# Kernel optimization log

Hardware: AMD Instinct MI355X
Metric: run time of the kernel (lower is better)

The kernel has to match this reference:

```python
import jax, jax.numpy as jnp
import numpy as np

H = 768   # config.hidden_size
B = 1024  # batch
S = 256   # attention context length
C1, C2, C3 = 202, 183, 11  # num_class for crit, law, time


def setup_inputs() -> dict:
    key = jax.random.key(0)
    ks = jax.random.split(key, 18)
    sd = 1.0 / np.sqrt(H)
    def u(k, shape):
        return jax.random.uniform(k, shape, jnp.float32, -sd, sd)
    return {
        "x": jax.random.normal(ks[0], (B, H), jnp.float32),
        "attn": jax.random.normal(ks[1], (B, S, H), jnp.float32),
        # 3 LSTMCells (tasks crit, law, time), stacked
        "Wih": u(ks[2], (3, 4 * H, H)),
        "Whh": u(ks[3], (3, 4 * H, H)),
        "bih": u(ks[4], (3, 4 * H)),
        "bhh": u(ks[5], (3, 4 * H)),
        # edge (2->3) hidden/cell state Linear (only edge whose FC is reached)
        "hfc_W": u(ks[6], (H, H)), "hfc_b": u(ks[7], (H,)),
        "cfc_W": u(ks[8], (H, H)), "cfc_b": u(ks[9], (H,)),
        # midfc per task
        "midfc_W": u(ks[10], (3, H, H)), "midfc_b": u(ks[11], (3, H)),
        # outfc per task (distinct class counts)
        "out1_W": u(ks[12], (C1, H)), "out1_b": u(ks[13], (C1,)),
        "out2_W": u(ks[14], (C2, H)), "out2_b": u(ks[15], (C2,)),
        "out3_W": u(ks[16], (C3, H)), "out3_b": u(ks[17], (C3,)),
    }


def _lstm_cell(x, h, c, Wih, Whh, bih, bhh):
    # torch nn.LSTMCell: gate order i, f, g, o
    gates = x @ Wih.T + bih + h @ Whh.T + bhh
    i, f, g, o = jnp.split(gates, 4, axis=-1)
    c_new = jax.nn.sigmoid(f) * c + jax.nn.sigmoid(i) * jnp.tanh(g)
    h_new = jax.nn.sigmoid(o) * jnp.tanh(c_new)
    return h_new, c_new


def _attend(h, attn):
    # Attention: ratio = softmax(bmm(attn, h)); result = bmm(attn^T, ratio)
    w = jax.nn.softmax(jnp.einsum('bsh,bh->bs', attn, h), axis=1)
    return jnp.einsum('bsh,bs->bh', attn, w)


def _head(h, mW, mb, oW, ob):
    # more_fc=True: outfc(relu(midfc(h)))
    return jax.nn.relu(h @ mW.T + mb) @ oW.T + ob


def reference(x, attn, Wih, Whh, bih, bhh, hfc_W, hfc_b, cfc_W, cfc_b,
              midfc_W, midfc_b, out1_W, out1_b, out2_W, out2_b, out3_W, out3_b):
    # graph "[(1 2),(1 3),(2 3)]": edges 1->2, 1->3, 2->3; initial hidden_list all zero.
    z = jnp.zeros_like(x)
    # task 1 (crit): runs on zero state; first-touch sets hidden[2]=hidden[3]=(h1,c1)
    h1, c1 = _lstm_cell(x, z, z, Wih[0], Whh[0], bih[0], bhh[0])
    # task 2 (law): state = (h1, c1)
    h2, c2 = _lstm_cell(x, h1, c1, Wih[1], Whh[1], bih[1], bhh[1])
    # edge 2->3 applies the per-edge Linear and accumulates into hidden[3]
    hp3 = h1 + h2 @ hfc_W.T + hfc_b
    cp3 = c1 + c2 @ cfc_W.T + cfc_b
    # task 3 (time)
    h3, c3 = _lstm_cell(x, hp3, cp3, Wih[2], Whh[2], bih[2], bhh[2])
    # attention over encoder context, per task head
    a1 = _attend(h1, attn)
    a2 = _attend(h2, attn)
    a3 = _attend(h3, attn)
    o1 = _head(a1, midfc_W[0], midfc_b[0], out1_W, out1_b)
    o2 = _head(a2, midfc_W[1], midfc_b[1], out2_W, out2_b)
    o3 = _head(a3, midfc_W[2], midfc_b[2], out3_W, out3_b)
    return (o1, o2, o3)
```

## Files before the change

### kernel.cpp

```cpp
#include <hip/hip_runtime.h>


typedef unsigned short u16;
typedef _Float16       f16x8 __attribute__((ext_vector_type(8)));
typedef float          f32x4 __attribute__((ext_vector_type(4)));

#define SWZ(r) ((((r) + ((r) >> 2))) & 3)

__device__ __forceinline__ u16 f2h(float f) {
  _Float16 h = (_Float16)f;
  return __builtin_bit_cast(u16, h);
}
__device__ __forceinline__ float sigm(float x) { return 1.f / (1.f + __expf(-x)); }
__device__ __forceinline__ float ftanh(float x) { return 1.f - 2.f / (__expf(2.f * x) + 1.f); }

__device__ __forceinline__ void gld16(const u16* g, u16* l) {
  __builtin_amdgcn_global_load_lds(
      (const __attribute__((address_space(1))) unsigned int*)(g),
      (__attribute__((address_space(3))) unsigned int*)(l),
      16, 0, 0);
}

struct GJob {
  const u16* A; const u16* W;
  float* outf; u16* outh;
  const float* bias; const float* bias2; const float* addend;
  int N; int ldc; int relu;
};
struct GArgs { GJob j[3]; };

__global__ __launch_bounds__(256)
void gemm_k(GArgs P, int K)
{
  const GJob jb = P.j[blockIdx.z];
  const int bn0 = blockIdx.x * 128;
  if (bn0 >= jb.N) return;
  const int bm0 = blockIdx.y * 64;

  __shared__ __align__(16) u16 As[2][64 * 32];
  __shared__ __align__(16) u16 Bs[2][128 * 32];

  const int tid = threadIdx.x, lane = tid & 63, wv = tid >> 6;

  const int ra  = tid >> 2,        csa  = (tid & 3) ^ SWZ(ra);
  const int rb0 = tid >> 2,        csb0 = (tid & 3) ^ SWZ(rb0);
  const int rb1 = (tid >> 2) + 64, csb1 = (tid & 3) ^ SWZ(rb1);
  int wr0 = bn0 + rb0; if (wr0 >= jb.N) wr0 = jb.N - 1;
  int wr1 = bn0 + rb1; if (wr1 >= jb.N) wr1 = jb.N - 1;
  const u16* gA  = jb.A + (size_t)(bm0 + ra) * K + csa * 8;
  const u16* gB0 = jb.W + (size_t)wr0 * K + csb0 * 8;
  const u16* gB1 = jb.W + (size_t)wr1 * K + csb1 * 8;

  const int frow = lane & 15, fsl = lane >> 4;

  f32x4 acc[8];
#pragma unroll
  for (int n = 0; n < 8; ++n) acc[n] = (f32x4){0.f, 0.f, 0.f, 0.f};

  const int NT = K >> 5;
  gld16(gA,  &As[0][wv * 512]);
  gld16(gB0, &Bs[0][wv * 512]);
  gld16(gB1, &Bs[0][2048 + wv * 512]);
  __syncthreads();

  for (int it = 0; it < NT; ++it) {
    const int cur = it & 1, nxt = cur ^ 1;
    if (it + 1 < NT) {
      const int k0 = (it + 1) * 32;
      gld16(gA + k0,  &As[nxt][wv * 512]);
      gld16(gB0 + k0, &Bs[nxt][wv * 512]);
      gld16(gB1 + k0, &Bs[nxt][2048 + wv * 512]);
    }
    f16x8 ah, bh[8];
    {
      const int ar = wv * 16 + frow;
      ah = *(const f16x8*)(&As[cur][ar * 32 + ((fsl ^ SWZ(ar)) * 8)]);
    }
#pragma unroll
    for (int n = 0; n < 8; ++n) {
      const int br = n * 16 + frow;
      bh[n] = *(const f16x8*)(&Bs[cur][br * 32 + ((fsl ^ SWZ(br)) * 8)]);
    }
#pragma unroll
    for (int n = 0; n < 8; ++n)
      acc[n] = __builtin_amdgcn_mfma_f32_16x16x32_f16(ah, bh[n], acc[n], 0, 0, 0);
    __syncthreads();
  }

  const int rb = (lane >> 4) * 4;
  const int cc = lane & 15;
#pragma unroll
  for (int n = 0; n < 8; ++n) {
    const int col = bn0 + n * 16 + cc;
    if (col >= jb.N) continue;
    float bv = 0.f;
    if (jb.bias)  bv += jb.bias[col];
    if (jb.bias2) bv += jb.bias2[col];
    const int row0 = bm0 + wv * 16 + rb;
#pragma unroll
    for (int r = 0; r < 4; ++r) {
      const int row = row0 + r;
      float v = acc[n][r] + bv;
      if (jb.addend) v += jb.addend[(size_t)row * jb.ldc + col];
      if (jb.relu)   v = fmaxf(v, 0.f);
      if (jb.outf)   jb.outf[(size_t)row * jb.ldc + col] = v;
      if (jb.outh)   jb.outh[(size_t)row * jb.ldc + col] = f2h(v);
    }
  }
}

__global__ __launch_bounds__(256)
void cell_k(const u16* __restrict__ A, const u16* __restrict__ W,
            const float* __restrict__ bi, const float* __restrict__ bh_,
            const float* __restrict__ addend, int lda,
            const float* __restrict__ cprev,
            float* __restrict__ hf, float* __restrict__ cf,
            u16* __restrict__ hh, u16* __restrict__ ch, int K)
{
  const int bj0 = blockIdx.x * 32;
  const int bm0 = blockIdx.y * 64;

  __shared__ __align__(16) u16 As[2][64 * 32];
  __shared__ __align__(16) u16 Bs[2][128 * 32];

  const int tid = threadIdx.x, lane = tid & 63, wv = tid >> 6;

  const int ra  = tid >> 2,        csa  = (tid & 3) ^ SWZ(ra);
  const int rb0 = tid >> 2,        csb0 = (tid & 3) ^ SWZ(rb0);
  const int rb1 = (tid >> 2) + 64, csb1 = (tid & 3) ^ SWZ(rb1);
  const int wr0 = (rb0 >> 5) * 768 + bj0 + (rb0 & 31);
  const int wr1 = (rb1 >> 5) * 768 + bj0 + (rb1 & 31);
  const u16* gA  = A + (size_t)(bm0 + ra) * K + csa * 8;
  const u16* gB0 = W + (size_t)wr0 * K + csb0 * 8;
  const u16* gB1 = W + (size_t)wr1 * K + csb1 * 8;

  const int frow = lane & 15, fsl = lane >> 4;

  f32x4 acc[8];
#pragma unroll
  for (int n = 0; n < 8; ++n) acc[n] = (f32x4){0.f, 0.f, 0.f, 0.f};

  const int NT = K >> 5;
  gld16(gA,  &As[0][wv * 512]);
  gld16(gB0, &Bs[0][wv * 512]);
  gld16(gB1, &Bs[0][2048 + wv * 512]);
  __syncthreads();

  for (int it = 0; it < NT; ++it) {
    const int cur = it & 1, nxt = cur ^ 1;
    if (it + 1 < NT) {
      const int k0 = (it + 1) * 32;
      gld16(gA + k0,  &As[nxt][wv * 512]);
      gld16(gB0 + k0, &Bs[nxt][wv * 512]);
      gld16(gB1 + k0, &Bs[nxt][2048 + wv * 512]);
    }
    f16x8 ah, bh8[8];
    {
      const int ar = wv * 16 + frow;
      ah = *(const f16x8*)(&As[cur][ar * 32 + ((fsl ^ SWZ(ar)) * 8)]);
    }
#pragma unroll
    for (int n = 0; n < 8; ++n) {
      const int br = n * 16 + frow;
      bh8[n] = *(const f16x8*)(&Bs[cur][br * 32 + ((fsl ^ SWZ(br)) * 8)]);
    }
#pragma unroll
    for (int n = 0; n < 8; ++n)
      acc[n] = __builtin_amdgcn_mfma_f32_16x16x32_f16(ah, bh8[n], acc[n], 0, 0, 0);
    __syncthreads();
  }

  const int rb = (lane >> 4) * 4;
  const int cc = lane & 15;
#pragma unroll
  for (int jj = 0; jj < 2; ++jj) {
    const int j = bj0 + jj * 16 + cc;
    float b_i = 0.f, b_f = 0.f, b_g = 0.f, b_o = 0.f;
    if (bi) {
      b_i = bi[j]        + bh_[j];
      b_f = bi[768 + j]  + bh_[768 + j];
      b_g = bi[1536 + j] + bh_[1536 + j];
      b_o = bi[2304 + j] + bh_[2304 + j];
    }
    const int row0 = bm0 + wv * 16 + rb;
#pragma unroll
    for (int r = 0; r < 4; ++r) {
      const int row = row0 + r;
      float gi = acc[0 + jj][r] + b_i;
      float gf = acc[2 + jj][r] + b_f;
      float gg = acc[4 + jj][r] + b_g;
      float go = acc[6 + jj][r] + b_o;
      if (addend) {
        const float* ad = addend + (size_t)row * lda;
        gi += ad[j]; gf += ad[768 + j]; gg += ad[1536 + j]; go += ad[2304 + j];
      }
      float c = sigm(gi) * ftanh(gg);
      if (cprev) c += sigm(gf) * cprev[row * 768 + j];
      float h = sigm(go) * ftanh(c);
      if (hf) hf[row * 768 + j] = h;
      if (cf) cf[row * 768 + j] = c;
      if (hh) hh[row * 768 + j] = f2h(h);
      if (ch) ch[row * 768 + j] = f2h(c);
    }
  }
}

struct CvtArgs {
  const float* src[9];
  u16*         dst[9];
  int n[9];
  int pfx[10];
};

__global__ __launch_bounds__(256)
void cvt_k(CvtArgs a)
{
  int blk = blockIdx.x, s = 0;
  while (s < 8 && blk >= a.pfx[s + 1]) ++s;
  int idx = ((blk - a.pfx[s]) * 256 + (int)threadIdx.x) * 4;
  if (idx >= a.n[s]) return;
  float4 v = *(const float4*)(a.src[s] + idx);
  ushort4 h;
  h.x = f2h(v.x); h.y = f2h(v.y); h.z = f2h(v.z); h.w = f2h(v.w);
  *(ushort4*)(a.dst[s] + idx) = h;
}

__global__ __launch_bounds__(256)
void attn_k(const float* __restrict__ attn,
            const float* __restrict__ h1, const float* __restrict__ h2,
            const float* __restrict__ h3,
            u16* __restrict__ a1, u16* __restrict__ a2, u16* __restrict__ a3)
{
  const int b = blockIdx.x, tid = threadIdx.x;
  const int lane = tid & 63, wv = tid >> 6;
  __shared__ float accW[4][3][768];
  __shared__ float lsumW[4][3];

  const float* ab = attn + (size_t)b * 256 * 768;
  const int cb = lane * 4;

  float4 hh[3][3];
#pragma unroll
  for (int j = 0; j < 3; ++j) {
    hh[0][j] = *(const float4*)(h1 + b * 768 + j * 256 + cb);
    hh[1][j] = *(const float4*)(h2 + b * 768 + j * 256 + cb);
    hh[2][j] = *(const float4*)(h3 + b * 768 + j * 256 + cb);
  }

  float4 acc[3][3];
#pragma unroll
  for (int t3 = 0; t3 < 3; ++t3)
#pragma unroll
    for (int j = 0; j < 3; ++j) acc[t3][j] = (float4){0.f, 0.f, 0.f, 0.f};
  float lsum[3] = {0.f, 0.f, 0.f};

  const int row0 = wv * 64;
  for (int sub = 0; sub < 16; ++sub) {
    const float* rp = ab + (size_t)(row0 + sub * 4) * 768 + cb;
    float4 vv[4][3];
#pragma unroll
    for (int s = 0; s < 4; ++s)
#pragma unroll
      for (int j = 0; j < 3; ++j)
        vv[s][j] = *(const float4*)(rp + s * 768 + j * 256);

    float q[3][4];
#pragma unroll
    for (int t3 = 0; t3 < 3; ++t3)
#pragma unroll
      for (int s = 0; s < 4; ++s) {
        float d = 0.f;
#pragma unroll
        for (int j = 0; j < 3; ++j) {
          d = fmaf(vv[s][j].x, hh[t3][j].x, d);
          d = fmaf(vv[s][j].y, hh[t3][j].y, d);
          d = fmaf(vv[s][j].z, hh[t3][j].z, d);
          d = fmaf(vv[s][j].w, hh[t3][j].w, d);
        }
        q[t3][s] = d;
      }
#pragma unroll
    for (int t3 = 0; t3 < 3; ++t3)
#pragma unroll
      for (int s = 0; s < 4; ++s) {
#pragma unroll
        for (int d = 1; d < 64; d <<= 1)
          q[t3][s] += __shfl_xor(q[t3][s], d);
        q[t3][s] = __expf(q[t3][s]);
      }
#pragma unroll
    for (int t3 = 0; t3 < 3; ++t3)
#pragma unroll
      for (int s = 0; s < 4; ++s) {
        const float p = q[t3][s];
        lsum[t3] += p;
#pragma unroll
        for (int j = 0; j < 3; ++j) {
          acc[t3][j].x = fmaf(p, vv[s][j].x, acc[t3][j].x);
          acc[t3][j].y = fmaf(p, vv[s][j].y, acc[t3][j].y);
          acc[t3][j].z = fmaf(p, vv[s][j].z, acc[t3][j].z);
          acc[t3][j].w = fmaf(p, vv[s][j].w, acc[t3][j].w);
        }
      }
  }

#pragma unroll
  for (int t3 = 0; t3 < 3; ++t3)
#pragma unroll
    for (int j = 0; j < 3; ++j)
      *(float4*)(&accW[wv][t3][j * 256 + cb]) = acc[t3][j];
  if (lane == 0) {
#pragma unroll
    for (int t3 = 0; t3 < 3; ++t3) lsumW[wv][t3] = lsum[t3];
  }
  __syncthreads();

  float ltot[3];
#pragma unroll
  for (int t3 = 0; t3 < 3; ++t3)
    ltot[t3] = lsumW[0][t3] + lsumW[1][t3] + lsumW[2][t3] + lsumW[3][t3];
  u16* outs[3] = { a1, a2, a3 };
#pragma unroll
  for (int cc = 0; cc < 3; ++cc) {
    const int c = tid + cc * 256;
#pragma unroll
    for (int t3 = 0; t3 < 3; ++t3) {
      float s = accW[0][t3][c] + accW[1][t3][c] + accW[2][t3][c] + accW[3][t3][c];
      outs[t3][b * 768 + c] = f2h(s / ltot[t3]);
    }
  }
}

extern "C" void kernel_launch(void* const* d_in, const int* in_sizes, int n_in,
                              void* d_out, int out_size, void* d_ws, size_t ws_size,
                              hipStream_t stream)
{
  const float* x    = (const float*)d_in[0];
  const float* attn = (const float*)d_in[1];
  const float* Wih  = (const float*)d_in[2];
  const float* Whh  = (const float*)d_in[3];
  const float* bih  = (const float*)d_in[4];
  const float* bhh  = (const float*)d_in[5];
  const float* hfcW = (const float*)d_in[6];
  const float* hfcb = (const float*)d_in[7];
  const float* cfcW = (const float*)d_in[8];
  const float* cfcb = (const float*)d_in[9];
  const float* midW = (const float*)d_in[10];
  const float* midb = (const float*)d_in[11];
  const float* o1W  = (const float*)d_in[12];
  const float* o1b  = (const float*)d_in[13];
  const float* o2W  = (const float*)d_in[14];
  const float* o2b  = (const float*)d_in[15];
  const float* o3W  = (const float*)d_in[16];
  const float* o3b  = (const float*)d_in[17];
  float* out = (float*)d_out;
  char*  ws  = (char*)d_ws;

  float* Gpre = (float*)(ws + 0);
  float* h1f  = (float*)(ws + 25165824);
  float* c1f  = (float*)(ws + 28311552);
  float* h2f  = (float*)(ws + 31457280);
  float* cp3f = (float*)(ws + 34603008);
  float* h3f  = (float*)(ws + 37748736);
  u16*   xh   = (u16*)(ws + 40894464);
  u16*   Wihh = (u16*)(ws + 42467328);
  u16*   Whhh = (u16*)(ws + 56623104);
  u16*   hfch = (u16*)(ws + 66060288);
  u16*   cfch = (u16*)(ws + 67239936);
  u16*   midh = (u16*)(ws + 68419584);
  u16*   o1h  = (u16*)(ws + 71958528);
  u16*   o2h  = (u16*)(ws + 72268800);
  u16*   o3h  = (u16*)(ws + 72549888);
  u16*   h1h  = (u16*)(ws + 72566784);
  u16*   h2h  = (u16*)(ws + 74139648);
  u16*   c2h  = (u16*)(ws + 75712512);
  u16*   hp3h = (u16*)(ws + 77285376);
  u16*   a1h  = (u16*)(ws + 78858240);
  u16*   a2h  = (u16*)(ws + 80431104);
  u16*   a3h  = (u16*)(ws + 82003968);
  u16*   m1h  = (u16*)(ws + 83576832);
  u16*   m2h  = (u16*)(ws + 85149696);
  u16*   m3h  = (u16*)(ws + 86722560);

  CvtArgs ca;
  const float* srcs[9] = { x, Wih, Whh + 2359296, hfcW, cfcW, midW, o1W, o2W, o3W };
  u16*         dsts[9] = { xh, Wihh, Whhh, hfch, cfch, midh, o1h, o2h, o3h };
  int ns[9] = { 786432, 7077888, 4718592, 589824, 589824, 1769472, 155136, 140544, 8448 };
  int pfx = 0;
  for (int i = 0; i < 9; ++i) {
    ca.src[i] = srcs[i]; ca.dst[i] = dsts[i]; ca.n[i] = ns[i];
    ca.pfx[i] = pfx; pfx += (ns[i] + 1023) / 1024;
  }
  ca.pfx[9] = pfx;
  cvt_k<<<pfx, 256, 0, stream>>>(ca);

  GArgs P;

  P = GArgs{};
  P.j[0] = { xh, Wihh + (size_t)3072 * 768, Gpre, nullptr,
             bih + 3072, bhh + 3072, nullptr, 6144, 6144, 0 };
  gemm_k<<<dim3(48, 16, 1), 256, 0, stream>>>(P, 768);

  cell_k<<<dim3(24, 16), 256, 0, stream>>>(xh, Wihh, bih, bhh,
      nullptr, 0, nullptr, h1f, c1f, h1h, nullptr, 768);

  cell_k<<<dim3(24, 16), 256, 0, stream>>>(h1h, Whhh, nullptr, nullptr,
      Gpre, 6144, c1f, h2f, nullptr, h2h, c2h, 768);

  P = GArgs{};
  P.j[0] = { h2h, hfch, nullptr, hp3h, hfcb, nullptr, h1f, 768, 768, 0 };
  P.j[1] = { c2h, cfch, cp3f, nullptr, cfcb, nullptr, c1f, 768, 768, 0 };
  gemm_k<<<dim3(6, 16, 2), 256, 0, stream>>>(P, 768);

  cell_k<<<dim3(24, 16), 256, 0, stream>>>(hp3h, Whhh + 2359296, nullptr, nullptr,
      Gpre + 3072, 6144, cp3f, h3f, nullptr, nullptr, nullptr, 768);

  attn_k<<<1024, 256, 0, stream>>>(attn, h1f, h2f, h3f, a1h, a2h, a3h);

  P = GArgs{};
  P.j[0] = { a1h, midh,           nullptr, m1h, midb,        nullptr, nullptr, 768, 768, 1 };
  P.j[1] = { a2h, midh +  589824, nullptr, m2h, midb +  768, nullptr, nullptr, 768, 768, 1 };
  P.j[2] = { a3h, midh + 1179648, nullptr, m3h, midb + 1536, nullptr, nullptr, 768, 768, 1 };
  gemm_k<<<dim3(6, 16, 3), 256, 0, stream>>>(P, 768);

  P = GArgs{};
  P.j[0] = { m1h, o1h, out,          nullptr, o1b, nullptr, nullptr, 202, 202, 0 };
  P.j[1] = { m2h, o2h, out + 206848, nullptr, o2b, nullptr, nullptr, 183, 183, 0 };
  P.j[2] = { m3h, o3h, out + 394240, nullptr, o3b, nullptr, nullptr,  11,  11, 0 };
  gemm_k<<<dim3(2, 16, 3), 256, 0, stream>>>(P, 768);

  (void)in_sizes; (void)n_in; (void)out_size; (void)ws_size;
}
```

Baseline: 348.9 us.

## Fuse input and recurrent GEMMs into cell kernels with 4-stage LDS pipeline

Removes the separate precomputed x@Wih gate GEMM for tasks 2 and 3. Each cell kernel now accumulates both x@Wih and h@Whh over a concatenated K of 1536, which avoids writing and re-reading a 25 MB fp32 gate buffer. The K loop in both the GEMM and cell kernels moves from double buffering to a 4-buffer LDS ring with three tiles in flight, using explicit vmcnt waits and raw barriers. The cost is more LDS per block (48 KB), which may reduce occupancy, and the cell kernels for tasks 2 and 3 now do twice the K work each.

```diff
diff --git a/kernel.cpp b/kernel.cpp
--- a/kernel.cpp
+++ b/kernel.cpp
@@ -6,6 +6,8 @@
 typedef float          f32x4 __attribute__((ext_vector_type(4)));
 
 #define SWZ(r) ((((r) + ((r) >> 2))) & 3)
+#define VMCNT(N) asm volatile("s_waitcnt vmcnt(" #N ")" ::: "memory")
+#define KBAR()  do { __builtin_amdgcn_s_barrier(); __builtin_amdgcn_sched_barrier(0); } while (0)
 
 __device__ __forceinline__ u16 f2h(float f) {
   _Float16 h = (_Float16)f;
@@ -20,6 +22,54 @@
       (__attribute__((address_space(3))) unsigned int*)(l),
       16, 0, 0);
 }
+
+struct KP { const u16 *pA1, *pA2, *pW1_0, *pW2_0, *pW1_1, *pW2_1; };
+
+__device__ __forceinline__ void stage_tile(const KP& kp, int kt, int ntA,
+                                           u16* Asb, u16* Bsb, int wv) {
+  const bool s1 = (kt < ntA);
+  const int off = (s1 ? kt : kt - ntA) * 32;
+  gld16((s1 ? kp.pA1  : kp.pA2 ) + off, Asb + wv * 512);
+  gld16((s1 ? kp.pW1_0 : kp.pW2_0) + off, Bsb + wv * 512);
+  gld16((s1 ? kp.pW1_1 : kp.pW2_1) + off, Bsb + 2048 + wv * 512);
+}
+
+__device__ __forceinline__ void compute_tile(const u16* Asb, const u16* Bsb,
+                                             int wv, int frow, int fsl, f32x4* acc) {
+  const int ar = wv * 16 + frow;
+  f16x8 ah = *(const f16x8*)(Asb + ar * 32 + ((fsl ^ SWZ(ar)) * 8));
+  f16x8 bh[8];
+#pragma unroll
+  for (int n = 0; n < 8; ++n) {
+    const int br = n * 16 + frow;
+    bh[n] = *(const f16x8*)(Bsb + br * 32 + ((fsl ^ SWZ(br)) * 8));
+  }
+#pragma unroll
+  for (int n = 0; n < 8; ++n)
+    acc[n] = __builtin_amdgcn_mfma_f32_16x16x32_f16(ah, bh[n], acc[n], 0, 0, 0);
+}
+
+#define KLOOP(kp, ntA, NT, As, Bs, wv, frow, fsl, acc)                          \
+  do {                                                                          \
+    stage_tile(kp, 0, ntA, As, Bs, wv);                                         \
+    stage_tile(kp, 1, ntA, As + 2048, Bs + 4096, wv);                           \
+    stage_tile(kp, 2, ntA, As + 4096, Bs + 8192, wv);                           \
+    for (int t = 0; t < NT - 2; ++t) {                                          \
+      VMCNT(6); KBAR();                                                         \
+      const int cb = t & 3;                                                     \
+      compute_tile(As + cb * 2048, Bs + cb * 4096, wv, frow, fsl, acc);         \
+      if (t + 3 < NT) {                                                         \
+        const int sb = (t + 3) & 3;                                             \
+        stage_tile(kp, t + 3, ntA, As + sb * 2048, Bs + sb * 4096, wv);         \
+      }                                                                         \
+    }                                                                           \
+    VMCNT(3); KBAR();                                                           \
+    compute_tile(As + ((NT - 2) & 3) * 2048, Bs + ((NT - 2) & 3) * 4096,        \
+                 wv, frow, fsl, acc);                                           \
+    VMCNT(0); KBAR();                                                           \
+    compute_tile(As + ((NT - 1) & 3) * 2048, Bs + ((NT - 1) & 3) * 4096,        \
+                 wv, frow, fsl, acc);                                           \
+  } while (0)
 
 struct GJob {
   const u16* A; const u16* W;
@@ -30,62 +80,35 @@
 struct GArgs { GJob j[3]; };
 
 __global__ __launch_bounds__(256)
-void gemm_k(GArgs P, int K)
+void gemm_k(GArgs P)
 {
   const GJob jb = P.j[blockIdx.z];
   const int bn0 = blockIdx.x * 128;
   if (bn0 >= jb.N) return;
   const int bm0 = blockIdx.y * 64;
 
-  __shared__ __align__(16) u16 As[2][64 * 32];
-  __shared__ __align__(16) u16 Bs[2][128 * 32];
+  __shared__ __align__(16) u16 As[4 * 64 * 32];
+  __shared__ __align__(16) u16 Bs[4 * 128 * 32];
 
   const int tid = threadIdx.x, lane = tid & 63, wv = tid >> 6;
+  const int frow = lane & 15, fsl = lane >> 4;
 
   const int ra  = tid >> 2,        csa  = (tid & 3) ^ SWZ(ra);
   const int rb0 = tid >> 2,        csb0 = (tid & 3) ^ SWZ(rb0);
   const int rb1 = (tid >> 2) + 64, csb1 = (tid & 3) ^ SWZ(rb1);
   int wr0 = bn0 + rb0; if (wr0 >= jb.N) wr0 = jb.N - 1;
   int wr1 = bn0 + rb1; if (wr1 >= jb.N) wr1 = jb.N - 1;
-  const u16* gA  = jb.A + (size_t)(bm0 + ra) * K + csa * 8;
-  const u16* gB0 = jb.W + (size_t)wr0 * K + csb0 * 8;
-  const u16* gB1 = jb.W + (size_t)wr1 * K + csb1 * 8;
-
-  const int frow = lane & 15, fsl = lane >> 4;
+
+  KP kp;
+  kp.pA1 = kp.pA2 = jb.A + (size_t)(bm0 + ra) * 768 + csa * 8;
+  kp.pW1_0 = kp.pW2_0 = jb.W + (size_t)wr0 * 768 + csb0 * 8;
+  kp.pW1_1 = kp.pW2_1 = jb.W + (size_t)wr1 * 768 + csb1 * 8;
 
   f32x4 acc[8];
 #pragma unroll
   for (int n = 0; n < 8; ++n) acc[n] = (f32x4){0.f, 0.f, 0.f, 0.f};
 
-  const int NT = K >> 5;
-  gld16(gA,  &As[0][wv * 512]);
-  gld16(gB0, &Bs[0][wv * 512]);
-  gld16(gB1, &Bs[0][2048 + wv * 512]);
-  __syncthreads();
-
-  for (int it = 0; it < NT; ++it) {
-    const int cur = it & 1, nxt = cur ^ 1;
-    if (it + 1 < NT) {
-      const int k0 = (it + 1) * 32;
-      gld16(gA + k0,  &As[nxt][wv * 512]);
-      gld16(gB0 + k0, &Bs[nxt][wv * 512]);
-      gld16(gB1 + k0, &Bs[nxt][2048 + wv * 512]);
-    }
-    f16x8 ah, bh[8];
-    {
-      const int ar = wv * 16 + frow;
-      ah = *(const f16x8*)(&As[cur][ar * 32 + ((fsl ^ SWZ(ar)) * 8)]);
-    }
-#pragma unroll
-    for (int n = 0; n < 8; ++n) {
-      const int br = n * 16 + frow;
-      bh[n] = *(const f16x8*)(&Bs[cur][br * 32 + ((fsl ^ SWZ(br)) * 8)]);
-    }
-#pragma unroll
-    for (int n = 0; n < 8; ++n)
-      acc[n] = __builtin_amdgcn_mfma_f32_16x16x32_f16(ah, bh[n], acc[n], 0, 0, 0);
-    __syncthreads();
-  }
+  KLOOP(kp, 24, 24, As, Bs, wv, frow, fsl, acc);
 
   const int rb = (lane >> 4) * 4;
   const int cc = lane & 15;
@@ -110,78 +133,51 @@
 }
 
 __global__ __launch_bounds__(256)
-void cell_k(const u16* __restrict__ A, const u16* __restrict__ W,
+void cell_k(const u16* __restrict__ A1, const u16* __restrict__ A2,
+            const u16* __restrict__ W1, const u16* __restrict__ W2,
             const float* __restrict__ bi, const float* __restrict__ bh_,
-            const float* __restrict__ addend, int lda,
             const float* __restrict__ cprev,
             float* __restrict__ hf, float* __restrict__ cf,
-            u16* __restrict__ hh, u16* __restrict__ ch, int K)
+            u16* __restrict__ hh, u16* __restrict__ ch, int NT)
 {
   const int bj0 = blockIdx.x * 32;
   const int bm0 = blockIdx.y * 64;
 
-  __shared__ __align__(16) u16 As[2][64 * 32];
-  __shared__ __align__(16) u16 Bs[2][128 * 32];
+  __shared__ __align__(16) u16 As[4 * 64 * 32];
+  __shared__ __align__(16) u16 Bs[4 * 128 * 32];
 
   const int tid = threadIdx.x, lane = tid & 63, wv = tid >> 6;
+  const int frow = lane & 15, fsl = lane >> 4;
 
   const int ra  = tid >> 2,        csa  = (tid & 3) ^ SWZ(ra);
   const int rb0 = tid >> 2,        csb0 = (tid & 3) ^ SWZ(rb0);
   const int rb1 = (tid >> 2) + 64, csb1 = (tid & 3) ^ SWZ(rb1);
   const int wr0 = (rb0 >> 5) * 768 + bj0 + (rb0 & 31);
   const int wr1 = (rb1 >> 5) * 768 + bj0 + (rb1 & 31);
-  const u16* gA  = A + (size_t)(bm0 + ra) * K + csa * 8;
-  const u16* gB0 = W + (size_t)wr0 * K + csb0 * 8;
-  const u16* gB1 = W + (size_t)wr1 * K + csb1 * 8;
-
-  const int frow = lane & 15, fsl = lane >> 4;
+
+  KP kp;
+  kp.pA1  = A1 + (size_t)(bm0 + ra) * 768 + csa * 8;
+  kp.pA2  = A2 + (size_t)(bm0 + ra) * 768 + csa * 8;
+  kp.pW1_0 = W1 + (size_t)wr0 * 768 + csb0 * 8;
+  kp.pW2_0 = W2 + (size_t)wr0 * 768 + csb0 * 8;
+  kp.pW1_1 = W1 + (size_t)wr1 * 768 + csb1 * 8;
+  kp.pW2_1 = W2 + (size_t)wr1 * 768 + csb1 * 8;
 
   f32x4 acc[8];
 #pragma unroll
   for (int n = 0; n < 8; ++n) acc[n] = (f32x4){0.f, 0.f, 0.f, 0.f};
 
-  const int NT = K >> 5;
-  gld16(gA,  &As[0][wv * 512]);
-  gld16(gB0, &Bs[0][wv * 512]);
-  gld16(gB1, &Bs[0][2048 + wv * 512]);
-  __syncthreads();
-
-  for (int it = 0; it < NT; ++it) {
-    const int cur = it & 1, nxt = cur ^ 1;
-    if (it + 1 < NT) {
-      const int k0 = (it + 1) * 32;
-      gld16(gA + k0,  &As[nxt][wv * 512]);
-      gld16(gB0 + k0, &Bs[nxt][wv * 512]);
-      gld16(gB1 + k0, &Bs[nxt][2048 + wv * 512]);
-    }
-    f16x8 ah, bh8[8];
-    {
-      const int ar = wv * 16 + frow;
-      ah = *(const f16x8*)(&As[cur][ar * 32 + ((fsl ^ SWZ(ar)) * 8)]);
-    }
-#pragma unroll
-    for (int n = 0; n < 8; ++n) {
-      const int br = n * 16 + frow;
-      bh8[n] = *(const f16x8*)(&Bs[cur][br * 32 + ((fsl ^ SWZ(br)) * 8)]);
-    }
-#pragma unroll
-    for (int n = 0; n < 8; ++n)
-      acc[n] = __builtin_amdgcn_mfma_f32_16x16x32_f16(ah, bh8[n], acc[n], 0, 0, 0);
-    __syncthreads();
-  }
+  KLOOP(kp, 24, NT, As, Bs, wv, frow, fsl, acc);
 
   const int rb = (lane >> 4) * 4;
   const int cc = lane & 15;
 #pragma unroll
   for (int jj = 0; jj < 2; ++jj) {
     const int j = bj0 + jj * 16 + cc;
-    float b_i = 0.f, b_f = 0.f, b_g = 0.f, b_o = 0.f;
-    if (bi) {
-      b_i = bi[j]        + bh_[j];
-      b_f = bi[768 + j]  + bh_[768 + j];
-      b_g = bi[1536 + j] + bh_[1536 + j];
-      b_o = bi[2304 + j] + bh_[2304 + j];
-    }
+    const float b_i = bi[j]        + bh_[j];
+    const float b_f = bi[768 + j]  + bh_[768 + j];
+    const float b_g = bi[1536 + j] + bh_[1536 + j];
+    const float b_o = bi[2304 + j] + bh_[2304 + j];
     const int row0 = bm0 + wv * 16 + rb;
 #pragma unroll
     for (int r = 0; r < 4; ++r) {
@@ -190,10 +186,6 @@
       float gf = acc[2 + jj][r] + b_f;
       float gg = acc[4 + jj][r] + b_g;
       float go = acc[6 + jj][r] + b_o;
-      if (addend) {
-        const float* ad = addend + (size_t)row * lda;
-        gi += ad[j]; gf += ad[768 + j]; gg += ad[1536 + j]; go += ad[2304 + j];
-      }
       float c = sigm(gi) * ftanh(gg);
       if (cprev) c += sigm(gf) * cprev[row * 768 + j];
       float h = sigm(go) * ftanh(c);
@@ -356,31 +348,30 @@
   float* out = (float*)d_out;
   char*  ws  = (char*)d_ws;
 
-  float* Gpre = (float*)(ws + 0);
-  float* h1f  = (float*)(ws + 25165824);
-  float* c1f  = (float*)(ws + 28311552);
-  float* h2f  = (float*)(ws + 31457280);
-  float* cp3f = (float*)(ws + 34603008);
-  float* h3f  = (float*)(ws + 37748736);
-  u16*   xh   = (u16*)(ws + 40894464);
-  u16*   Wihh = (u16*)(ws + 42467328);
-  u16*   Whhh = (u16*)(ws + 56623104);
-  u16*   hfch = (u16*)(ws + 66060288);
-  u16*   cfch = (u16*)(ws + 67239936);
-  u16*   midh = (u16*)(ws + 68419584);
-  u16*   o1h  = (u16*)(ws + 71958528);
-  u16*   o2h  = (u16*)(ws + 72268800);
-  u16*   o3h  = (u16*)(ws + 72549888);
-  u16*   h1h  = (u16*)(ws + 72566784);
-  u16*   h2h  = (u16*)(ws + 74139648);
-  u16*   c2h  = (u16*)(ws + 75712512);
-  u16*   hp3h = (u16*)(ws + 77285376);
-  u16*   a1h  = (u16*)(ws + 78858240);
-  u16*   a2h  = (u16*)(ws + 80431104);
-  u16*   a3h  = (u16*)(ws + 82003968);
-  u16*   m1h  = (u16*)(ws + 83576832);
-  u16*   m2h  = (u16*)(ws + 85149696);
-  u16*   m3h  = (u16*)(ws + 86722560);
+  float* h1f  = (float*)(ws + 0);
+  float* c1f  = (float*)(ws + 3145728);
+  float* h2f  = (float*)(ws + 6291456);
+  float* cp3f = (float*)(ws + 9437184);
+  float* h3f  = (float*)(ws + 12582912);
+  u16*   xh   = (u16*)(ws + 15728640);
+  u16*   Wihh = (u16*)(ws + 17301504);
+  u16*   Whhh = (u16*)(ws + 31457280);
+  u16*   hfch = (u16*)(ws + 40894464);
+  u16*   cfch = (u16*)(ws + 42074112);
+  u16*   midh = (u16*)(ws + 43253760);
+  u16*   o1h  = (u16*)(ws + 46792704);
+  u16*   o2h  = (u16*)(ws + 47102976);
+  u16*   o3h  = (u16*)(ws + 47384064);
+  u16*   h1h  = (u16*)(ws + 47400960);
+  u16*   h2h  = (u16*)(ws + 48973824);
+  u16*   c2h  = (u16*)(ws + 50546688);
+  u16*   hp3h = (u16*)(ws + 52119552);
+  u16*   a1h  = (u16*)(ws + 53692416);
+  u16*   a2h  = (u16*)(ws + 55265280);
+  u16*   a3h  = (u16*)(ws + 56838144);
+  u16*   m1h  = (u16*)(ws + 58411008);
+  u16*   m2h  = (u16*)(ws + 59983872);
+  u16*   m3h  = (u16*)(ws + 61556736);
 
   CvtArgs ca;
   const float* srcs[9] = { x, Wih, Whh + 2359296, hfcW, cfcW, midW, o1W, o2W, o3W };
@@ -396,24 +387,21 @@
 
   GArgs P;
 
-  P = GArgs{};
-  P.j[0] = { xh, Wihh + (size_t)3072 * 768, Gpre, nullptr,
-             bih + 3072, bhh + 3072, nullptr, 6144, 6144, 0 };
-  gemm_k<<<dim3(48, 16, 1), 256, 0, stream>>>(P, 768);
-
-  cell_k<<<dim3(24, 16), 256, 0, stream>>>(xh, Wihh, bih, bhh,
-      nullptr, 0, nullptr, h1f, c1f, h1h, nullptr, 768);
-
-  cell_k<<<dim3(24, 16), 256, 0, stream>>>(h1h, Whhh, nullptr, nullptr,
-      Gpre, 6144, c1f, h2f, nullptr, h2h, c2h, 768);
+  cell_k<<<dim3(24, 16), 256, 0, stream>>>(xh, xh, Wihh, Wihh,
+      bih, bhh, nullptr, h1f, c1f, h1h, nullptr, 24);
+
+  cell_k<<<dim3(24, 16), 256, 0, stream>>>(xh, h1h,
+      Wihh + (size_t)3072 * 768, Whhh,
+      bih + 3072, bhh + 3072, c1f, h2f, nullptr, h2h, c2h, 48);
 
   P = GArgs{};
   P.j[0] = { h2h, hfch, nullptr, hp3h, hfcb, nullptr, h1f, 768, 768, 0 };
   P.j[1] = { c2h, cfch, cp3f, nullptr, cfcb, nullptr, c1f, 768, 768, 0 };
-  gemm_k<<<dim3(6, 16, 2), 256, 0, stream>>>(P, 768);
-
-  cell_k<<<dim3(24, 16), 256, 0, stream>>>(hp3h, Whhh + 2359296, nullptr, nullptr,
-      Gpre + 3072, 6144, cp3f, h3f, nullptr, nullptr, nullptr, 768);
+  gemm_k<<<dim3(6, 16, 2), 256, 0, stream>>>(P);
+
+  cell_k<<<dim3(24, 16), 256, 0, stream>>>(xh, hp3h,
+      Wihh + (size_t)6144 * 768, Whhh + 2359296,
+      bih + 6144, bhh + 6144, cp3f, h3f, nullptr, nullptr, nullptr, 48);
 
   attn_k<<<1024, 256, 0, stream>>>(attn, h1f, h2f, h3f, a1h, a2h, a3h);
 
@@ -421,13 +409,13 @@
   P.j[0] = { a1h, midh,           nullptr, m1h, midb,        nullptr, nullptr, 768, 768, 1 };
   P.j[1] = { a2h, midh +  589824, nullptr, m2h, midb +  768, nullptr, nullptr, 768, 768, 1 };
   P.j[2] = { a3h, midh + 1179648, nullptr, m3h, midb + 1536, nullptr, nullptr, 768, 768, 1 };
-  gemm_k<<<dim3(6, 16, 3), 256, 0, stream>>>(P, 768);
+  gemm_k<<<dim3(6, 16, 3), 256, 0, stream>>>(P);
 
   P = GArgs{};
   P.j[0] = { m1h, o1h, out,          nullptr, o1b, nullptr, nullptr, 202, 202, 0 };
   P.j[1] = { m2h, o2h, out + 206848, nullptr, o2b, nullptr, nullptr, 183, 183, 0 };
   P.j[2] = { m3h, o3h, out + 394240, nullptr, o3b, nullptr, nullptr,  11,  11, 0 };
-  gemm_k<<<dim3(2, 16, 3), 256, 0, stream>>>(P, 768);
+  gemm_k<<<dim3(2, 16, 3), 256, 0, stream>>>(P);
 
   (void)in_sizes; (void)n_in; (void)out_size; (void)ws_size;
 }
```

Result: faster. 323.1 us (-7.4%).

## Deepen GEMM pipeline to four LDS stages and fuse first-stage kernels

Applied to the files above, without the earlier changes.

The shared GEMM main loop now uses a four-buffer LDS ring with three tiles in flight. It waits with explicit vmcnt counters and raw barriers instead of double buffering with a __syncthreads per tile. The conversion kernel is split in two: x and Wih are converted first, then one fused kernel runs cell 1, the Wih gate precompute GEMM and the remaining weight conversions as separate block ranges. This removes launches and overlaps conversion with compute. K is now hardcoded to 768 and LDS use per block doubles, which may lower occupancy.

```diff
diff --git a/kernel.cpp b/kernel.cpp
--- a/kernel.cpp
+++ b/kernel.cpp
@@ -6,6 +6,8 @@
 typedef float          f32x4 __attribute__((ext_vector_type(4)));
 
 #define SWZ(r) ((((r) + ((r) >> 2))) & 3)
+#define VMCNT(N) asm volatile("s_waitcnt vmcnt(" #N ")" ::: "memory")
+#define KBAR()  do { __builtin_amdgcn_s_barrier(); __builtin_amdgcn_sched_barrier(0); } while (0)
 
 __device__ __forceinline__ u16 f2h(float f) {
   _Float16 h = (_Float16)f;
@@ -19,6 +21,54 @@
       (const __attribute__((address_space(1))) unsigned int*)(g),
       (__attribute__((address_space(3))) unsigned int*)(l),
       16, 0, 0);
+}
+
+struct KP { const u16 *pA, *pW0, *pW1; };
+
+__device__ __forceinline__ void stage_tile(const KP& kp, int kt,
+                                           u16* Asb, u16* Bsb, int wv) {
+  const int off = kt * 32;
+  gld16(kp.pA  + off, Asb + wv * 512);
+  gld16(kp.pW0 + off, Bsb + wv * 512);
+  gld16(kp.pW1 + off, Bsb + 2048 + wv * 512);
+}
+
+__device__ __forceinline__ void compute_tile(const u16* Asb, const u16* Bsb,
+                                             int wv, int frow, int fsl, f32x4* acc) {
+  const int ar = wv * 16 + frow;
+  f16x8 ah = *(const f16x8*)(Asb + ar * 32 + ((fsl ^ SWZ(ar)) * 8));
+  f16x8 bh[8];
+#pragma unroll
+  for (int n = 0; n < 8; ++n) {
+    const int br = n * 16 + frow;
+    bh[n] = *(const f16x8*)(Bsb + br * 32 + ((fsl ^ SWZ(br)) * 8));
+  }
+#pragma unroll
+  for (int n = 0; n < 8; ++n)
+    acc[n] = __builtin_amdgcn_mfma_f32_16x16x32_f16(ah, bh[n], acc[n], 0, 0, 0);
+}
+
+__device__ __forceinline__ void kloop(const KP& kp, u16* As, u16* Bs,
+                                      int wv, int frow, int fsl, f32x4* acc) {
+  const int NT = 24;
+  stage_tile(kp, 0, As,        Bs,        wv);
+  stage_tile(kp, 1, As + 2048, Bs + 4096, wv);
+  stage_tile(kp, 2, As + 4096, Bs + 8192, wv);
+  for (int t = 0; t < NT - 2; ++t) {
+    VMCNT(6); KBAR();
+    const int cb = t & 3;
+    compute_tile(As + cb * 2048, Bs + cb * 4096, wv, frow, fsl, acc);
+    if (t + 3 < NT) {
+      const int sb = (t + 3) & 3;
+      stage_tile(kp, t + 3, As + sb * 2048, Bs + sb * 4096, wv);
+    }
+  }
+  VMCNT(3); KBAR();
+  compute_tile(As + ((NT - 2) & 3) * 2048, Bs + ((NT - 2) & 3) * 4096,
+               wv, frow, fsl, acc);
+  VMCNT(0); KBAR();
+  compute_tile(As + ((NT - 1) & 3) * 2048, Bs + ((NT - 1) & 3) * 4096,
+               wv, frow, fsl, acc);
 }
 
 struct GJob {
@@ -27,65 +77,30 @@
   const float* bias; const float* bias2; const float* addend;
   int N; int ldc; int relu;
 };
-struct GArgs { GJob j[3]; };
-
-__global__ __launch_bounds__(256)
-void gemm_k(GArgs P, int K)
-{
-  const GJob jb = P.j[blockIdx.z];
-  const int bn0 = blockIdx.x * 128;
+
+__device__ __forceinline__ void run_gemm(const GJob& jb, int bx, int by,
+                                         u16* As, u16* Bs, int tid) {
+  const int bn0 = bx * 128;
   if (bn0 >= jb.N) return;
-  const int bm0 = blockIdx.y * 64;
-
-  __shared__ __align__(16) u16 As[2][64 * 32];
-  __shared__ __align__(16) u16 Bs[2][128 * 32];
-
-  const int tid = threadIdx.x, lane = tid & 63, wv = tid >> 6;
+  const int bm0 = by * 64;
+  const int lane = tid & 63, wv = tid >> 6;
+  const int frow = lane & 15, fsl = lane >> 4;
 
   const int ra  = tid >> 2,        csa  = (tid & 3) ^ SWZ(ra);
-  const int rb0 = tid >> 2,        csb0 = (tid & 3) ^ SWZ(rb0);
   const int rb1 = (tid >> 2) + 64, csb1 = (tid & 3) ^ SWZ(rb1);
-  int wr0 = bn0 + rb0; if (wr0 >= jb.N) wr0 = jb.N - 1;
+  int wr0 = bn0 + ra;  if (wr0 >= jb.N) wr0 = jb.N - 1;
   int wr1 = bn0 + rb1; if (wr1 >= jb.N) wr1 = jb.N - 1;
-  const u16* gA  = jb.A + (size_t)(bm0 + ra) * K + csa * 8;
-  const u16* gB0 = jb.W + (size_t)wr0 * K + csb0 * 8;
-  const u16* gB1 = jb.W + (size_t)wr1 * K + csb1 * 8;
-
-  const int frow = lane & 15, fsl = lane >> 4;
+
+  KP kp;
+  kp.pA  = jb.A + (size_t)(bm0 + ra) * 768 + csa * 8;
+  kp.pW0 = jb.W + (size_t)wr0 * 768 + csa * 8;
+  kp.pW1 = jb.W + (size_t)wr1 * 768 + csb1 * 8;
 
   f32x4 acc[8];
 #pragma unroll
   for (int n = 0; n < 8; ++n) acc[n] = (f32x4){0.f, 0.f, 0.f, 0.f};
 
-  const int NT = K >> 5;
-  gld16(gA,  &As[0][wv * 512]);
-  gld16(gB0, &Bs[0][wv * 512]);
-  gld16(gB1, &Bs[0][2048 + wv * 512]);
-  __syncthreads();
-
-  for (int it = 0; it < NT; ++it) {
-    const int cur = it & 1, nxt = cur ^ 1;
-    if (it + 1 < NT) {
-      const int k0 = (it + 1) * 32;
-      gld16(gA + k0,  &As[nxt][wv * 512]);
-      gld16(gB0 + k0, &Bs[nxt][wv * 512]);
-      gld16(gB1 + k0, &Bs[nxt][2048 + wv * 512]);
-    }
-    f16x8 ah, bh[8];
-    {
-      const int ar = wv * 16 + frow;
-      ah = *(const f16x8*)(&As[cur][ar * 32 + ((fsl ^ SWZ(ar)) * 8)]);
-    }
-#pragma unroll
-    for (int n = 0; n < 8; ++n) {
-      const int br = n * 16 + frow;
-      bh[n] = *(const f16x8*)(&Bs[cur][br * 32 + ((fsl ^ SWZ(br)) * 8)]);
-    }
-#pragma unroll
-    for (int n = 0; n < 8; ++n)
-      acc[n] = __builtin_amdgcn_mfma_f32_16x16x32_f16(ah, bh[n], acc[n], 0, 0, 0);
-    __syncthreads();
-  }
+  kloop(kp, As, Bs, wv, frow, fsl, acc);
 
   const int rb = (lane >> 4) * 4;
   const int cc = lane & 15;
@@ -109,66 +124,33 @@
   }
 }
 
-__global__ __launch_bounds__(256)
-void cell_k(const u16* __restrict__ A, const u16* __restrict__ W,
-            const float* __restrict__ bi, const float* __restrict__ bh_,
-            const float* __restrict__ addend, int lda,
-            const float* __restrict__ cprev,
-            float* __restrict__ hf, float* __restrict__ cf,
-            u16* __restrict__ hh, u16* __restrict__ ch, int K)
-{
-  const int bj0 = blockIdx.x * 32;
-  const int bm0 = blockIdx.y * 64;
-
-  __shared__ __align__(16) u16 As[2][64 * 32];
-  __shared__ __align__(16) u16 Bs[2][128 * 32];
-
-  const int tid = threadIdx.x, lane = tid & 63, wv = tid >> 6;
+__device__ __forceinline__ void run_cell(const u16* A, const u16* W,
+                                         const float* bi, const float* bh_,
+                                         const float* addend,
+                                         const float* cprev,
+                                         float* hf, float* cf, u16* hh, u16* ch,
+                                         int bx, int by,
+                                         u16* As, u16* Bs, int tid) {
+  const int bj0 = bx * 32;
+  const int bm0 = by * 64;
+  const int lane = tid & 63, wv = tid >> 6;
+  const int frow = lane & 15, fsl = lane >> 4;
 
   const int ra  = tid >> 2,        csa  = (tid & 3) ^ SWZ(ra);
-  const int rb0 = tid >> 2,        csb0 = (tid & 3) ^ SWZ(rb0);
   const int rb1 = (tid >> 2) + 64, csb1 = (tid & 3) ^ SWZ(rb1);
-  const int wr0 = (rb0 >> 5) * 768 + bj0 + (rb0 & 31);
+  const int wr0 = (ra >> 5) * 768 + bj0 + (ra & 31);
   const int wr1 = (rb1 >> 5) * 768 + bj0 + (rb1 & 31);
-  const u16* gA  = A + (size_t)(bm0 + ra) * K + csa * 8;
-  const u16* gB0 = W + (size_t)wr0 * K + csb0 * 8;
-  const u16* gB1 = W + (size_t)wr1 * K + csb1 * 8;
-
-  const int frow = lane & 15, fsl = lane >> 4;
+
+  KP kp;
+  kp.pA  = A + (size_t)(bm0 + ra) * 768 + csa * 8;
+  kp.pW0 = W + (size_t)wr0 * 768 + csa * 8;
+  kp.pW1 = W + (size_t)wr1 * 768 + csb1 * 8;
 
   f32x4 acc[8];
 #pragma unroll
   for (int n = 0; n < 8; ++n) acc[n] = (f32x4){0.f, 0.f, 0.f, 0.f};
 
-  const int NT = K >> 5;
-  gld16(gA,  &As[0][wv * 512]);
-  gld16(gB0, &Bs[0][wv * 512]);
-  gld16(gB1, &Bs[0][2048 + wv * 512]);
-  __syncthreads();
-
-  for (int it = 0; it < NT; ++it) {
-    const int cur = it & 1, nxt = cur ^ 1;
-    if (it + 1 < NT) {
-      const int k0 = (it + 1) * 32;
-      gld16(gA + k0,  &As[nxt][wv * 512]);
-      gld16(gB0 + k0, &Bs[nxt][wv * 512]);
-      gld16(gB1 + k0, &Bs[nxt][2048 + wv * 512]);
-    }
-    f16x8 ah, bh8[8];
-    {
-      const int ar = wv * 16 + frow;
-      ah = *(const f16x8*)(&As[cur][ar * 32 + ((fsl ^ SWZ(ar)) * 8)]);
-    }
-#pragma unroll
-    for (int n = 0; n < 8; ++n) {
-      const int br = n * 16 + frow;
-      bh8[n] = *(const f16x8*)(&Bs[cur][br * 32 + ((fsl ^ SWZ(br)) * 8)]);
-    }
-#pragma unroll
-    for (int n = 0; n < 8; ++n)
-      acc[n] = __builtin_amdgcn_mfma_f32_16x16x32_f16(ah, bh8[n], acc[n], 0, 0, 0);
-    __syncthreads();
-  }
+  kloop(kp, As, Bs, wv, frow, fsl, acc);
 
   const int rb = (lane >> 4) * 4;
   const int cc = lane & 15;
@@ -191,7 +173,7 @@
       float gg = acc[4 + jj][r] + b_g;
       float go = acc[6 + jj][r] + b_o;
       if (addend) {
-        const float* ad = addend + (size_t)row * lda;
+        const float* ad = addend + (size_t)row * 6144;
         gi += ad[j]; gf += ad[768 + j]; gg += ad[1536 + j]; go += ad[2304 + j];
       }
       float c = sigm(gi) * ftanh(gg);
@@ -205,24 +187,79 @@
   }
 }
 
-struct CvtArgs {
-  const float* src[9];
-  u16*         dst[9];
-  int n[9];
-  int pfx[10];
+__device__ __forceinline__ void cvt_seg(const float* s, u16* d, int n4,
+                                        int gtid, int nthr) {
+  for (int i = gtid; i < n4; i += nthr) {
+    float4 v = ((const float4*)s)[i];
+    ushort4 h;
+    h.x = f2h(v.x); h.y = f2h(v.y); h.z = f2h(v.z); h.w = f2h(v.w);
+    ((ushort4*)d)[i] = h;
+  }
+}
+
+__global__ __launch_bounds__(256)
+void cvt0_k(const float* x, u16* xh, const float* Wih, u16* Wihh)
+{
+  const int g = blockIdx.x * 256 + threadIdx.x, N = 2048 * 256;
+  cvt_seg(x,   xh,   196608,  g, N);
+  cvt_seg(Wih, Wihh, 1769472, g, N);
+}
+
+struct K1P {
+  const u16 *xh, *Wihh;
+  const float *bih, *bhh;
+  float *h1f, *c1f; u16* h1h;
+  float* Gpre;
+  const float *Whh, *hfcW, *cfcW, *midW, *o1W, *o2W, *o3W;
+  u16 *Whhh, *hfch, *cfch, *midh, *o1h, *o2h, *o3h;
 };
 
 __global__ __launch_bounds__(256)
-void cvt_k(CvtArgs a)
-{
-  int blk = blockIdx.x, s = 0;
-  while (s < 8 && blk >= a.pfx[s + 1]) ++s;
-  int idx = ((blk - a.pfx[s]) * 256 + (int)threadIdx.x) * 4;
-  if (idx >= a.n[s]) return;
-  float4 v = *(const float4*)(a.src[s] + idx);
-  ushort4 h;
-  h.x = f2h(v.x); h.y = f2h(v.y); h.z = f2h(v.z); h.w = f2h(v.w);
-  *(ushort4*)(a.dst[s] + idx) = h;
+void k1_k(K1P p)
+{
+  __shared__ __align__(16) u16 As[4 * 64 * 32];
+  __shared__ __align__(16) u16 Bs[4 * 128 * 32];
+  const int blk = blockIdx.x, tid = threadIdx.x;
+
+  if (blk < 384) {
+    run_cell(p.xh, p.Wihh, p.bih, p.bhh, nullptr, nullptr,
+             p.h1f, p.c1f, p.h1h, nullptr, blk % 24, blk / 24, As, Bs, tid);
+  } else if (blk < 1152) {
+    const int r = blk - 384;
+    GJob jb = { p.xh, p.Wihh + (size_t)3072 * 768, p.Gpre, nullptr,
+                p.bih + 3072, p.bhh + 3072, nullptr, 6144, 6144, 0 };
+    run_gemm(jb, r % 48, r / 48, As, Bs, tid);
+  } else {
+    const int g = (blk - 1152) * 256 + tid, N = 384 * 256;
+    cvt_seg(p.Whh + 2359296, p.Whhh, 1179648, g, N);
+    cvt_seg(p.hfcW, p.hfch, 147456, g, N);
+    cvt_seg(p.cfcW, p.cfch, 147456, g, N);
+    cvt_seg(p.midW, p.midh, 442368, g, N);
+    cvt_seg(p.o1W,  p.o1h,  38784,  g, N);
+    cvt_seg(p.o2W,  p.o2h,  35136,  g, N);
+    cvt_seg(p.o3W,  p.o3h,  2112,   g, N);
+  }
+}
+
+__global__ __launch_bounds__(256)
+void cell_k(const u16* __restrict__ A, const u16* __restrict__ W,
+            const float* __restrict__ addend, const float* __restrict__ cprev,
+            float* hf, float* cf, u16* hh, u16* ch)
+{
+  __shared__ __align__(16) u16 As[4 * 64 * 32];
+  __shared__ __align__(16) u16 Bs[4 * 128 * 32];
+  run_cell(A, W, nullptr, nullptr, addend, cprev, hf, cf, hh, ch,
+           blockIdx.x, blockIdx.y, As, Bs, threadIdx.x);
+}
+
+struct GArgs { GJob j[3]; };
+
+__global__ __launch_bounds__(256)
+void gemm_k(GArgs P)
+{
+  __shared__ __align__(16) u16 As[4 * 64 * 32];
+  __shared__ __align__(16) u16 Bs[4 * 128 * 32];
+  run_gemm(P.j[blockIdx.z], blockIdx.x, blockIdx.y, As, Bs, threadIdx.x);
 }
 
 __global__ __launch_bounds__(256)
@@ -236,7 +273,7 @@
   __shared__ float accW[4][3][768];
   __shared__ float lsumW[4][3];
 
-  const float* ab = attn + (size_t)b * 256 * 768;
+  const float* ab = attn + (size_t)b * 196608;
   const int cb = lane * 4;
 
   float4 hh[3][3];
@@ -292,14 +329,14 @@
     for (int t3 = 0; t3 < 3; ++t3)
 #pragma unroll
       for (int s = 0; s < 4; ++s) {
-        const float p = q[t3][s];
-        lsum[t3] += p;
+        const float pw = q[t3][s];
+        lsum[t3] += pw;
 #pragma unroll
         for (int j = 0; j < 3; ++j) {
-          acc[t3][j].x = fmaf(p, vv[s][j].x, acc[t3][j].x);
-          acc[t3][j].y = fmaf(p, vv[s][j].y, acc[t3][j].y);
-          acc[t3][j].z = fmaf(p, vv[s][j].z, acc[t3][j].z);
-          acc[t3][j].w = fmaf(p, vv[s][j].w, acc[t3][j].w);
+          acc[t3][j].x = fmaf(pw, vv[s][j].x, acc[t3][j].x);
+          acc[t3][j].y = fmaf(pw, vv[s][j].y, acc[t3][j].y);
+          acc[t3][j].z = fmaf(pw, vv[s][j].z, acc[t3][j].z);
+          acc[t3][j].w = fmaf(pw, vv[s][j].w, acc[t3][j].w);
         }
       }
   }
@@ -382,38 +419,29 @@
   u16*   m2h  = (u16*)(ws + 85149696);
   u16*   m3h  = (u16*)(ws + 86722560);
 
-  CvtArgs ca;
-  const float* srcs[9] = { x, Wih, Whh + 2359296, hfcW, cfcW, midW, o1W, o2W, o3W };
-  u16*         dsts[9] = { xh, Wihh, Whhh, hfch, cfch, midh, o1h, o2h, o3h };
-  int ns[9] = { 786432, 7077888, 4718592, 589824, 589824, 1769472, 155136, 140544, 8448 };
-  int pfx = 0;
-  for (int i = 0; i < 9; ++i) {
-    ca.src[i] = srcs[i]; ca.dst[i] = dsts[i]; ca.n[i] = ns[i];
-    ca.pfx[i] = pfx; pfx += (ns[i] + 1023) / 1024;
-  }
-  ca.pfx[9] = pfx;
-  cvt_k<<<pfx, 256, 0, stream>>>(ca);
+  cvt0_k<<<2048, 256, 0, stream>>>(x, xh, Wih, Wihh);
+
+  K1P p1;
+  p1.xh = xh; p1.Wihh = Wihh; p1.bih = bih; p1.bhh = bhh;
+  p1.h1f = h1f; p1.c1f = c1f; p1.h1h = h1h; p1.Gpre = Gpre;
+  p1.Whh = Whh; p1.hfcW = hfcW; p1.cfcW = cfcW; p1.midW = midW;
+  p1.o1W = o1W; p1.o2W = o2W; p1.o3W = o3W;
+  p1.Whhh = Whhh; p1.hfch = hfch; p1.cfch = cfch; p1.midh = midh;
+  p1.o1h = o1h; p1.o2h = o2h; p1.o3h = o3h;
+  k1_k<<<1536, 256, 0, stream>>>(p1);
+
+  cell_k<<<dim3(24, 16), 256, 0, stream>>>(h1h, Whhh, Gpre, c1f,
+                                           h2f, nullptr, h2h, c2h);
 
   GArgs P;
-
-  P = GArgs{};
-  P.j[0] = { xh, Wihh + (size_t)3072 * 768, Gpre, nullptr,
-             bih + 3072, bhh + 3072, nullptr, 6144, 6144, 0 };
-  gemm_k<<<dim3(48, 16, 1), 256, 0, stream>>>(P, 768);
-
-  cell_k<<<dim3(24, 16), 256, 0, stream>>>(xh, Wihh, bih, bhh,
-      nullptr, 0, nullptr, h1f, c1f, h1h, nullptr, 768);
-
-  cell_k<<<dim3(24, 16), 256, 0, stream>>>(h1h, Whhh, nullptr, nullptr,
-      Gpre, 6144, c1f, h2f, nullptr, h2h, c2h, 768);
-
   P = GArgs{};
   P.j[0] = { h2h, hfch, nullptr, hp3h, hfcb, nullptr, h1f, 768, 768, 0 };
   P.j[1] = { c2h, cfch, cp3f, nullptr, cfcb, nullptr, c1f, 768, 768, 0 };
-  gemm_k<<<dim3(6, 16, 2), 256, 0, stream>>>(P, 768);
-
-  cell_k<<<dim3(24, 16), 256, 0, stream>>>(hp3h, Whhh + 2359296, nullptr, nullptr,
-      Gpre + 3072, 6144, cp3f, h3f, nullptr, nullptr, nullptr, 768);
+  P.j[2] = P.j[1];
+  gemm_k<<<dim3(6, 16, 2), 256, 0, stream>>>(P);
+
+  cell_k<<<dim3(24, 16), 256, 0, stream>>>(hp3h, Whhh + 2359296, Gpre + 3072,
+                                           cp3f, h3f, nullptr, nullptr, nullptr);
 
   attn_k<<<1024, 256, 0, stream>>>(attn, h1f, h2f, h3f, a1h, a2h, a3h);
 
@@ -421,13 +449,13 @@
   P.j[0] = { a1h, midh,           nullptr, m1h, midb,        nullptr, nullptr, 768, 768, 1 };
   P.j[1] = { a2h, midh +  589824, nullptr, m2h, midb +  768, nullptr, nullptr, 768, 768, 1 };
   P.j[2] = { a3h, midh + 1179648, nullptr, m3h, midb + 1536, nullptr, nullptr, 768, 768, 1 };
-  gemm_k<<<dim3(6, 16, 3), 256, 0, stream>>>(P, 768);
+  gemm_k<<<dim3(6, 16, 3), 256, 0, stream>>>(P);
 
   P = GArgs{};
   P.j[0] = { m1h, o1h, out,          nullptr, o1b, nullptr, nullptr, 202, 202, 0 };
   P.j[1] = { m2h, o2h, out + 206848, nullptr, o2b, nullptr, nullptr, 183, 183, 0 };
   P.j[2] = { m3h, o3h, out + 394240, nullptr, o3b, nullptr, nullptr,  11,  11, 0 };
-  gemm_k<<<dim3(2, 16, 3), 256, 0, stream>>>(P, 768);
+  gemm_k<<<dim3(2, 16, 3), 256, 0, stream>>>(P);
 
   (void)in_sizes; (void)n_in; (void)out_size; (void)ws_size;
 }
```

Result: faster. 318.6 us (-8.7%).
